# Kernel optimization log

Hardware: AMD Instinct MI355X
Metric: run time of the kernel (lower is better)

Reference implementation:

```python
import jax, jax.numpy as jnp
import numpy as np

N = 1_000_000        # points
V = 200_000          # occupied voxels
B = 4                # scans per batch
NUM_CLASSES = 20
DIM_POINT = 4
EPS = 1e-5


def bn(x, g, b):
    # eval-mode BatchNorm1d with running_mean=0, running_var=1
    return x * (g / jnp.sqrt(1.0 + EPS)) + b


def _lin(key, fi, fo):
    # kaiming-normal init, bias-free Linear stored as [in, out]
    return jax.random.normal(key, (fi, fo), jnp.float32) * np.sqrt(2.0 / fi)


def setup_inputs() -> dict:
    key = jax.random.key(0)
    ks = jax.random.split(key, 20)
    batch_ids = (jnp.arange(N) * B // N).astype(jnp.float32)[:, None]
    coords = jax.random.normal(ks[0], (N, DIM_POINT), jnp.float32)
    points = jnp.concatenate([batch_ids, coords], axis=1)           # [N, 1+dim_point]
    pv_ids = jax.random.randint(ks[1], (N,), 0, V, jnp.int64)       # point -> voxel
    ones, zeros = jnp.ones, jnp.zeros
    return {
        'points': points, 'point_voxel_ids': pv_ids,
        # point encoder: 4->32->64->32, each Linear(no bias)+BN+ReLU
        'pe_w1': _lin(ks[2], DIM_POINT, 32), 'pe_g1': ones(32), 'pe_b1': zeros(32),
        'pe_w2': _lin(ks[3], 32, 64),        'pe_g2': ones(64), 'pe_b2': zeros(64),
        'pe_w3': _lin(ks[4], 64, 32),        'pe_g3': ones(32), 'pe_b3': zeros(32),
        # voxel encoder (SparseUnet simplified to per-voxel 32->32->32)
        've_w1': _lin(ks[5], 32, 32), 've_g1': ones(32), 've_b1': zeros(32),
        've_w2': _lin(ks[6], 32, 32), 've_g2': ones(32), 've_b2': zeros(32),
        # fusion encoder: 64->64
        'fu_w': _lin(ks[7], 64, 64), 'fu_g': ones(64), 'fu_b': zeros(64),
        # FlattenSELayer: 64 -> 64//16 -> 64 with biases
        'se_w1': _lin(ks[8], 64, 4),  'se_b1': zeros(4),
        'se_w2': _lin(ks[9], 4, 64),  'se_b2': zeros(64),
        # main classifier 64->32->num_classes
        'cls_w1': _lin(ks[10], 64, 32), 'cls_g1': ones(32), 'cls_b1': zeros(32),
        'cls_w2': _lin(ks[11], 32, NUM_CLASSES),
        # aux classifier 32->32->num_classes
        'aux_w1': _lin(ks[12], 32, 32), 'aux_g1': ones(32), 'aux_b1': zeros(32),
        'aux_w2': _lin(ks[13], 32, NUM_CLASSES),
    }


def reference(points, point_voxel_ids,
              pe_w1, pe_g1, pe_b1, pe_w2, pe_g2, pe_b2, pe_w3, pe_g3, pe_b3,
              ve_w1, ve_g1, ve_b1, ve_w2, ve_g2, ve_b2,
              fu_w, fu_g, fu_b, se_w1, se_b1, se_w2, se_b2,
              cls_w1, cls_g1, cls_b1, cls_w2,
              aux_w1, aux_g1, aux_b1, aux_w2):
    batch_ids = points[:, 0].astype(jnp.int32)
    pv = point_voxel_ids.astype(jnp.int32)
    x = points[:, 1:]
    # point encoder
    pf = jax.nn.relu(bn(x @ pe_w1, pe_g1, pe_b1))
    pf = jax.nn.relu(bn(pf @ pe_w2, pe_g2, pe_b2))
    pf = jax.nn.relu(bn(pf @ pe_w3, pe_g3, pe_b3))               # [N,32]
    # voxel_max_pooling: point -> voxel scatter-max (empty voxels -> 0)
    vox = jax.ops.segment_max(pf, pv, num_segments=V)
    vox = jnp.where(jnp.isfinite(vox), vox, 0.0)                 # [V,32]
    # voxel encoder (SparseUnet stand-in); v1 is the aux feature tap
    v1 = jax.nn.relu(bn(vox @ ve_w1, ve_g1, ve_b1))              # [V,32]
    vf = jax.nn.relu(bn(v1 @ ve_w2, ve_g2, ve_b2))               # [V,32]
    # voxel_to_point gather + fusion
    pvf = vf[pv]                                                  # [N,32]
    fused = jnp.concatenate([pvf, pf], axis=1)                   # [N,64]
    fused = jax.nn.relu(bn(fused @ fu_w, fu_g, fu_b))
    # FlattenSELayer: per-scan mean -> gate -> residual scale
    sums = jax.ops.segment_sum(fused, batch_ids, num_segments=B)
    cnts = jax.ops.segment_sum(jnp.ones((fused.shape[0], 1), fused.dtype), batch_ids, num_segments=B)
    mean = sums / jnp.maximum(cnts, 1.0)                         # [B,64]
    gate = jax.nn.sigmoid(jax.nn.relu(mean @ se_w1 + se_b1) @ se_w2 + se_b2)
    fused = fused + fused * gate[batch_ids]
    # heads (dropout is identity at inference)
    out = jax.nn.relu(bn(fused @ cls_w1, cls_g1, cls_b1)) @ cls_w2      # [N,C]
    aux_out = jax.nn.relu(bn(v1 @ aux_w1, aux_g1, aux_b1)) @ aux_w2     # [V,C]
    return out, aux_out
```

## Files before the change

### kernel.cpp

```cpp
#include <hip/hip_runtime.h>
#include <hip/hip_bf16.h>

#define NPTS 1000000
#define NVOX 200000
#define NCLS 20

typedef __hip_bfloat16 bf16;
typedef __attribute__((ext_vector_type(8))) short bf16x8_t;
typedef __attribute__((ext_vector_type(4))) float f32x4_t;
#define MFMA16(a, b, c) __builtin_amdgcn_mfma_f32_16x16x32_bf16(a, b, c, 0, 0, 0)

constexpr size_t L_PV   = 0;
constexpr size_t L_BID  = L_PV + NPTS;
constexpr size_t L_CNT  = L_BID + NPTS;
constexpr size_t L_BSUM = L_CNT + NVOX;
constexpr size_t L_BCNT = L_BSUM + 2048;
constexpr size_t L_GATE = L_BCNT + 4;
constexpr size_t L_OFFS = L_GATE + 256;
constexpr size_t L_BS1  = L_OFFS + NVOX;
constexpr size_t L_BB   = L_BS1 + 256;
constexpr size_t L_IDX  = L_BB + 256;
constexpr size_t L_IOR  = L_IDX + NPTS;
constexpr size_t L_W    = L_IOR + NPTS;
constexpr int O_PE1W = 0;      constexpr int O_PE1B = 128;
constexpr int O_PE2W = 160;    constexpr int O_PE2B = 2208;
constexpr int O_PE3W = 2272;   constexpr int O_PE3B = 4320;
constexpr int O_VE1W = 4352;   constexpr int O_VE1B = 5376;
constexpr int O_VE2W = 5408;   constexpr int O_VE2B = 6432;
constexpr int O_FUW  = 6464;   constexpr int O_FUB  = 10560;
constexpr int O_SE1W = 10624;  constexpr int O_SE1B = 10880;
constexpr int O_SE2W = 10884;  constexpr int O_SE2B = 11140;
constexpr int O_CLS1W = 11204; constexpr int O_CLS1B = 13252;
constexpr int O_CLS2W = 13284;
constexpr int O_AUX1W = 13924; constexpr int O_AUX1B = 14948;
constexpr int O_AUX2W = 14980;
constexpr int W_TOTAL = 15620;
constexpr size_t L_WT  = L_W + W_TOTAL;
constexpr int WT_FU = 0;
constexpr int WT_C1 = 4096;
constexpr int WT_C2 = 6144;
constexpr int WT_2H = 7168;
constexpr int WT_2L = 9216;
constexpr int WT_3H = 11264;
constexpr int WT_3L = 13312;
constexpr int WT_C1B = 15360;
constexpr int WT_U16 = 15360 + 8192;
constexpr size_t L_PFQ = L_WT + WT_U16 / 2;
constexpr size_t L_VFP = L_PFQ + (size_t)NPTS * 16;
static_assert((L_PFQ * 4) % 16 == 0, "pfq alignment");
static_assert((L_VFP * 4) % 16 == 0, "vfp alignment");

static __device__ __forceinline__ float b2f(bf16 v) { return __bfloat162float(v); }
static __device__ __forceinline__ float us2f(unsigned short u) { return __uint_as_float((unsigned)u << 16); }
static __device__ __forceinline__ unsigned short f2us(float f) {
    unsigned u = __float_as_uint(f);
    u += 0x7fffu + ((u >> 16) & 1u);
    return (unsigned short)(u >> 16);
}
static __device__ __forceinline__ unsigned pack2(float a, float b) {
    return (unsigned)f2us(a) | ((unsigned)f2us(b) << 16);
}
static __device__ __forceinline__ void unpack2(unsigned u, float& a, float& b) {
    a = __uint_as_float(u << 16);
    b = __uint_as_float(u & 0xffff0000u);
}
static __device__ __forceinline__ float rdf(const void* p, size_t idx, int fp32) {
    return fp32 ? ((const float*)p)[idx] : b2f(((const bf16*)p)[idx]);
}
static __device__ __forceinline__ int detect_fp32(const void* pts_raw) {
    const unsigned short* ptsu = (const unsigned short*)pts_raw;
    return (ptsu[1] == 0 && ptsu[11] == 0) ? 1 : 0;
}
static __device__ __forceinline__ int detect_i64(const void* pv_raw) {
    const unsigned* pvu = (const unsigned*)pv_raw;
    return (pvu[1] == 0 && pvu[3] == 0 && pvu[5] == 0 && pvu[7] == 0) ? 1 : 0;
}

template <int K, int M, bool RELU, bool BIAS>
static __device__ __forceinline__ void dense(const float* __restrict__ x, float* __restrict__ y,
                                             const float* __restrict__ w, const float* __restrict__ b) {
#pragma unroll
    for (int j = 0; j < M; ++j) {
        float a = BIAS ? b[j] : 0.f;
#pragma unroll
        for (int k = 0; k < K; ++k) a = fmaf(x[k], w[k * M + j], a);
        y[j] = RELU ? fmaxf(a, 0.f) : a;
    }
}

static __device__ __forceinline__ int block_excl_scan(int v, int t) {
    __shared__ int sh[2][256];
    int cur = 0;
    sh[0][t] = v; __syncthreads();
#pragma unroll
    for (int off = 1; off < 256; off <<= 1) {
        int val = sh[cur][t];
        if (t >= off) val += sh[cur][t - off];
        sh[cur ^ 1][t] = val; __syncthreads();
        cur ^= 1;
    }
    return sh[cur][t] - v;
}

struct WPtrs {
    const void *pe_w1, *pe_g1, *pe_b1, *pe_w2, *pe_g2, *pe_b2, *pe_w3, *pe_g3, *pe_b3;
    const void *ve_w1, *ve_g1, *ve_b1, *ve_w2, *ve_g2, *ve_b2;
    const void *fu_w, *fu_g, *fu_b;
    const void *se_w1, *se_b1, *se_w2, *se_b2;
    const void *cls_w1, *cls_g1, *cls_b1, *cls_w2;
    const void *aux_w1, *aux_g1, *aux_b1, *aux_w2;
};

static __device__ void foldw(float* d, const void* w, const void* g, int K, int M, int fp32) {
    const float INV = 0.9999950000374997f;
    for (int idx = threadIdx.x; idx < K * M; idx += 256)
        d[idx] = rdf(w, idx, fp32) * (rdf(g, idx % M, fp32) * INV);
}
static __device__ void cpv(float* d, const void* s, int n, int fp32) {
    for (int idx = threadIdx.x; idx < n; idx += 256) d[idx] = rdf(s, idx, fp32);
}

__global__ void k0_prep(WPtrs p, const void* __restrict__ pts_raw, float* __restrict__ W,
                        unsigned short* __restrict__ WT) {
    int f = detect_fp32(pts_raw);
    foldw(W + O_PE1W, p.pe_w1, p.pe_g1, 4, 32, f);   cpv(W + O_PE1B, p.pe_b1, 32, f);
    foldw(W + O_PE2W, p.pe_w2, p.pe_g2, 32, 64, f);  cpv(W + O_PE2B, p.pe_b2, 64, f);
    foldw(W + O_PE3W, p.pe_w3, p.pe_g3, 64, 32, f);  cpv(W + O_PE3B, p.pe_b3, 32, f);
    foldw(W + O_VE1W, p.ve_w1, p.ve_g1, 32, 32, f);  cpv(W + O_VE1B, p.ve_b1, 32, f);
    foldw(W + O_VE2W, p.ve_w2, p.ve_g2, 32, 32, f);  cpv(W + O_VE2B, p.ve_b2, 32, f);
    foldw(W + O_FUW,  p.fu_w,  p.fu_g,  64, 64, f);  cpv(W + O_FUB,  p.fu_b, 64, f);
    cpv(W + O_SE1W, p.se_w1, 256, f);  cpv(W + O_SE1B, p.se_b1, 4, f);
    cpv(W + O_SE2W, p.se_w2, 256, f);  cpv(W + O_SE2B, p.se_b2, 64, f);
    foldw(W + O_CLS1W, p.cls_w1, p.cls_g1, 64, 32, f); cpv(W + O_CLS1B, p.cls_b1, 32, f);
    cpv(W + O_CLS2W, p.cls_w2, 640, f);
    foldw(W + O_AUX1W, p.aux_w1, p.aux_g1, 32, 32, f); cpv(W + O_AUX1B, p.aux_b1, 32, f);
    cpv(W + O_AUX2W, p.aux_w2, 640, f);
    __syncthreads();
    unsigned short* wtfu = WT + WT_FU;
    unsigned short* wtc1 = WT + WT_C1;
    unsigned short* wtc2 = WT + WT_C2;
    unsigned short* wt2h = WT + WT_2H;
    unsigned short* wt2l = WT + WT_2L;
    unsigned short* wt3h = WT + WT_3H;
    unsigned short* wt3l = WT + WT_3L;
    for (int idx = threadIdx.x; idx < 4096; idx += 256) {
        int n = idx >> 6, k = idx & 63;
        wtfu[idx] = f2us(W[O_FUW + k * 64 + n]);
    }
    for (int idx = threadIdx.x; idx < 2048; idx += 256) {
        int n = idx >> 6, k = idx & 63;
        wtc1[idx] = f2us(W[O_CLS1W + k * 32 + n]);
    }
    for (int idx = threadIdx.x; idx < 1024; idx += 256) {
        int n = idx >> 5, k = idx & 31;
        wtc2[idx] = (n < NCLS) ? f2us(W[O_CLS2W + k * NCLS + n]) : (unsigned short)0;
    }
    for (int idx = threadIdx.x; idx < 2048; idx += 256) {
        int n = idx >> 5, k = idx & 31;
        float v = W[O_PE2W + k * 64 + n];
        unsigned short hi = f2us(v);
        wt2h[idx] = hi;
        wt2l[idx] = f2us(v - us2f(hi));
    }
    for (int idx = threadIdx.x; idx < 2048; idx += 256) {
        int n = idx >> 6, k = idx & 63;
        float v = W[O_PE3W + k * 32 + n];
        unsigned short hi = f2us(v);
        wt3h[idx] = hi;
        wt3l[idx] = f2us(v - us2f(hi));
    }
}

__global__ __launch_bounds__(256) void k_scan1(const int* __restrict__ cnt, int* __restrict__ bs) {
    int t = threadIdx.x;
    int base = blockIdx.x * 1024 + t * 4;
    int s = 0;
#pragma unroll
    for (int k = 0; k < 4; ++k) { int idx = base + k; if (idx < NVOX) s += cnt[idx]; }
    __shared__ int red[256];
    red[t] = s; __syncthreads();
    for (int off = 128; off > 0; off >>= 1) { if (t < off) red[t] += red[t + off]; __syncthreads(); }
    if (t == 0) bs[blockIdx.x] = red[0];
}

__global__ __launch_bounds__(256) void k_scan2(const int* __restrict__ bs, int* __restrict__ bb, int nb) {
    int t = threadIdx.x;
    int v = (t < nb) ? bs[t] : 0;
    int e = block_excl_scan(v, t);
    bb[t] = e;
}

__global__ __launch_bounds__(256) void k_scan3(const int* __restrict__ cnt, const int* __restrict__ bb,
                                               int* __restrict__ offs) {
    int t = threadIdx.x;
    int base = blockIdx.x * 1024 + t * 4;
    int c[4]; int s = 0;
#pragma unroll
    for (int k = 0; k < 4; ++k) { int idx = base + k; c[k] = (idx < NVOX) ? cnt[idx] : 0; s += c[k]; }
    int run = bb[blockIdx.x] + block_excl_scan(s, t);
#pragma unroll
    for (int k = 0; k < 4; ++k) {
        int idx = base + k;
        if (idx < NVOX) { offs[idx] = run; run += c[k]; }
    }
}

__global__ __launch_bounds__(256) void k1_fused(const void* __restrict__ pts_raw,
                                                const void* __restrict__ pv_raw,
                                                const float* __restrict__ W,
                                                const unsigned short* __restrict__ WT2H,
                                                const unsigned short* __restrict__ WT2L,
                                                const unsigned short* __restrict__ WT3H,
                                                const unsigned short* __restrict__ WT3L,
                                                int* __restrict__ pvN,
                                                int* __restrict__ bidN,
                                                int* __restrict__ cnt,
                                                float* __restrict__ bcnt,
                                                int* __restrict__ rank,
                                                uint4* __restrict__ pf_q) {
    __shared__ __align__(16) unsigned short hth[4][16][72];
    __shared__ __align__(16) unsigned short htl[4][16][72];
    __shared__ __align__(16) unsigned short pt[4][16][40];
    int t = threadIdx.x;
    int lane = t & 63, w = t >> 6;
    int m = lane & 15, quad = lane >> 4;
    int i0 = blockIdx.x * 256;
    int fp32 = detect_fp32(pts_raw), i64 = detect_i64(pv_raw);

    float w1[32], b1[8];
#pragma unroll
    for (int k = 0; k < 4; ++k)
#pragma unroll
        for (int j = 0; j < 8; ++j) w1[k * 8 + j] = W[O_PE1W + k * 32 + quad * 8 + j];
#pragma unroll
    for (int j = 0; j < 8; ++j) b1[j] = W[O_PE1B + quad * 8 + j];
    bf16x8_t b2h[4], b2l[4], b3h[2][2], b3l[2][2];
    float bias2[4], bias3[2];
#pragma unroll
    for (int tn = 0; tn < 4; ++tn) {
        b2h[tn] = *(const bf16x8_t*)(WT2H + (tn * 16 + m) * 32 + quad * 8);
        b2l[tn] = *(const bf16x8_t*)(WT2L + (tn * 16 + m) * 32 + quad * 8);
        bias2[tn] = W[O_PE2B + tn * 16 + m];
    }
#pragma unroll
    for (int tn = 0; tn < 2; ++tn) {
#pragma unroll
        for (int kh = 0; kh < 2; ++kh) {
            b3h[tn][kh] = *(const bf16x8_t*)(WT3H + (tn * 16 + m) * 64 + kh * 32 + quad * 8);
            b3l[tn][kh] = *(const bf16x8_t*)(WT3L + (tn * 16 + m) * 64 + kh * 32 + quad * 8);
        }
        bias3[tn] = W[O_PE3B + tn * 16 + m];
    }
    int nval = NPTS - i0; if (nval > 256) nval = 256;
    int ntiles = (nval - w * 64 >= 64) ? 4 : 0;

#pragma unroll 1
    for (int tt = 0; tt < ntiles; ++tt) {
        int rbase = i0 + w * 64 + tt * 16;
        int arow = rbase + m;
        float4 c;
        c.x = rdf(pts_raw, (size_t)arow * 5 + 1, fp32);
        c.y = rdf(pts_raw, (size_t)arow * 5 + 2, fp32);
        c.z = rdf(pts_raw, (size_t)arow * 5 + 3, fp32);
        c.w = rdf(pts_raw, (size_t)arow * 5 + 4, fp32);
        union { unsigned u[4]; bf16x8_t v; } ah, al;
#pragma unroll
        for (int pp = 0; pp < 4; ++pp) {
            unsigned hu = 0, lu = 0;
#pragma unroll
            for (int s = 0; s < 2; ++s) {
                int j = 2 * pp + s;
                float h = b1[j];
                h = fmaf(c.x, w1[0 * 8 + j], h);
                h = fmaf(c.y, w1[1 * 8 + j], h);
                h = fmaf(c.z, w1[2 * 8 + j], h);
                h = fmaf(c.w, w1[3 * 8 + j], h);
                h = fmaxf(h, 0.f);
                unsigned short hi = f2us(h);
                unsigned short lo = f2us(h - us2f(hi));
                hu |= (unsigned)hi << (16 * s);
                lu |= (unsigned)lo << (16 * s);
            }
            ah.u[pp] = hu; al.u[pp] = lu;
        }
#pragma unroll
        for (int tn = 0; tn < 4; ++tn) {
            f32x4_t acc = {0.f, 0.f, 0.f, 0.f};
            acc = MFMA16(ah.v, b2h[tn], acc);
            acc = MFMA16(ah.v, b2l[tn], acc);
            acc = MFMA16(al.v, b2h[tn], acc);
#pragma unroll
            for (int e = 0; e < 4; ++e) {
                float v = fmaxf(acc[e] + bias2[tn], 0.f);
                unsigned short hi = f2us(v);
                hth[w][quad * 4 + e][tn * 16 + m] = hi;
                htl[w][quad * 4 + e][tn * 16 + m] = f2us(v - us2f(hi));
            }
        }
        bf16x8_t x0h = *(const bf16x8_t*)&hth[w][m][quad * 8];
        bf16x8_t x1h = *(const bf16x8_t*)&hth[w][m][32 + quad * 8];
        bf16x8_t x0l = *(const bf16x8_t*)&htl[w][m][quad * 8];
        bf16x8_t x1l = *(const bf16x8_t*)&htl[w][m][32 + quad * 8];
#pragma unroll
        for (int tn = 0; tn < 2; ++tn) {
            f32x4_t acc = {0.f, 0.f, 0.f, 0.f};
            acc = MFMA16(x0h, b3h[tn][0], acc);
            acc = MFMA16(x1h, b3h[tn][1], acc);
            acc = MFMA16(x0h, b3l[tn][0], acc);
            acc = MFMA16(x1h, b3l[tn][1], acc);
            acc = MFMA16(x0l, b3h[tn][0], acc);
            acc = MFMA16(x1l, b3h[tn][1], acc);
#pragma unroll
            for (int e = 0; e < 4; ++e)
                pt[w][quad * 4 + e][tn * 16 + m] = f2us(fmaxf(acc[e] + bias3[tn], 0.f));
        }
        uint4 q = *(const uint4*)&pt[w][m][quad * 8];
        pf_q[(size_t)arow * 4 + quad] = q;
    }

    int i = i0 + t;
    bool valid = t < nval;
    int b = 0, rk = 0;
    if (valid) {
        b = (int)rdf(pts_raw, (size_t)i * 5, fp32);
        bidN[i] = b;
        int v = i64 ? (int)((const long long*)pv_raw)[i] : ((const int*)pv_raw)[i];
        pvN[i] = v;
        rk = atomicAdd(&cnt[v], 1);
    }
    __shared__ int sb0, sflag;
    if (t == 0) { sb0 = b; sflag = 1; }
    __syncthreads();
    if (valid && b != sb0) sflag = 0;
    __syncthreads();
    if (sflag) {
        if (t == 0) atomicAdd(&bcnt[sb0], (float)nval);
    } else if (valid) {
        atomicAdd(&bcnt[b], 1.f);
    }
    if (valid) rank[i] = rk;
}

__global__ __launch_bounds__(256) void k_sidx(const int* __restrict__ pv,
                                              const int* __restrict__ rank,
                                              const int* __restrict__ offs,
                                              int* __restrict__ idxs) {
    int i = blockIdx.x * 256 + threadIdx.x;
    if (i >= NPTS) return;
    idxs[offs[pv[i]] + rank[i]] = i;
}

__global__ __launch_bounds__(256) void k_voxmlp(const int* __restrict__ offs, const int* __restrict__ cnt,
                                                const int* __restrict__ idxs,
                                                const uint4* __restrict__ pf_q,
                                                const float* __restrict__ W,
                                                const void* __restrict__ pts_raw,
                                                uint4* __restrict__ vfp,
                                                void* __restrict__ outbase) {
    int v = blockIdx.x * 256 + threadIdx.x;
    if (v >= NVOX) return;
    int of32 = detect_fp32(pts_raw);
    float mx[32];
#pragma unroll
    for (int c = 0; c < 32; ++c) mx[c] = 0.f;
    int s = offs[v], n = cnt[v];
    for (int p = 0; p < n; ++p) {
        int j = idxs[s + p];
        size_t base = (size_t)j * 4;
#pragma unroll
        for (int t = 0; t < 4; ++t) {
            uint4 q = pf_q[base + t];
            float a, b;
            unpack2(q.x, a, b); mx[8*t+0] = fmaxf(mx[8*t+0], a); mx[8*t+1] = fmaxf(mx[8*t+1], b);
            unpack2(q.y, a, b); mx[8*t+2] = fmaxf(mx[8*t+2], a); mx[8*t+3] = fmaxf(mx[8*t+3], b);
            unpack2(q.z, a, b); mx[8*t+4] = fmaxf(mx[8*t+4], a); mx[8*t+5] = fmaxf(mx[8*t+5], b);
            unpack2(q.w, a, b); mx[8*t+6] = fmaxf(mx[8*t+6], a); mx[8*t+7] = fmaxf(mx[8*t+7], b);
        }
    }
    float v1[32], vf[32], a1[32], o[20];
    dense<32, 32, true, true>(mx, v1, W + O_VE1W, W + O_VE1B);
    dense<32, 32, true, true>(v1, vf, W + O_VE2W, W + O_VE2B);
    uint4 vq[4];
#pragma unroll
    for (int t = 0; t < 4; ++t)
        vq[t] = make_uint4(pack2(vf[8*t+0], vf[8*t+1]), pack2(vf[8*t+2], vf[8*t+3]),
                           pack2(vf[8*t+4], vf[8*t+5]), pack2(vf[8*t+6], vf[8*t+7]));
    for (int p = 0; p < n; ++p) {
        int j = idxs[s + p];
        uint4* d = vfp + (size_t)j * 4;
        d[0] = vq[0]; d[1] = vq[1]; d[2] = vq[2]; d[3] = vq[3];
    }
    dense<32, 32, true, true>(v1, a1, W + O_AUX1W, W + O_AUX1B);
    dense<32, 20, false, false>(a1, o, W + O_AUX2W, nullptr);
    if (of32) {
        float* auxf = (float*)outbase + (size_t)NPTS * NCLS + (size_t)v * NCLS;
#pragma unroll
        for (int t = 0; t < NCLS; ++t) __builtin_nontemporal_store(o[t], auxf + t);
    } else {
        unsigned* auxu = (unsigned*)((bf16*)outbase + (size_t)NPTS * NCLS);
#pragma unroll
        for (int t = 0; t < 10; ++t) __builtin_nontemporal_store(pack2(o[2*t], o[2*t+1]), auxu + (size_t)v * 10 + t);
    }
}

__global__ __launch_bounds__(256) void k3_mfma(const int* __restrict__ bid,
                                               const uint4* __restrict__ pf_q,
                                               const uint4* __restrict__ vfp,
                                               const float* __restrict__ W,
                                               const unsigned short* __restrict__ WTfu,
                                               float* __restrict__ bsum8) {
    __shared__ int sbid[256];
    __shared__ float red[4][64];
    __shared__ int sflag;
    int t = threadIdx.x;
    int i0 = blockIdx.x * 256;
    int nval = NPTS - i0; if (nval > 256) nval = 256;
    if (t < nval) sbid[t] = bid[i0 + t];
    if (t == 0) sflag = (bid[i0] == bid[i0 + nval - 1]) ? 1 : 0;

    int lane = t & 63, w = t >> 6;
    int m = lane & 15, quad = lane >> 4;
    bf16x8_t bw0[4], bw1[4];
    float bias[4];
#pragma unroll
    for (int tn = 0; tn < 4; ++tn) {
        bw0[tn] = *(const bf16x8_t*)(WTfu + (tn * 16 + m) * 64 + quad * 8);
        bw1[tn] = *(const bf16x8_t*)(WTfu + (tn * 16 + m) * 64 + 32 + quad * 8);
        bias[tn] = W[O_FUB + tn * 16 + m];
    }
    __syncthreads();
    int uni = sflag;
    int b0 = sbid[0];
    int rep = (blockIdx.x & 7) * 256;
    int ntiles = (nval - w * 64 >= 64) ? 4 : 0;

    float csum[4] = {0.f, 0.f, 0.f, 0.f};
#pragma unroll
    for (int tt = 0; tt < 4; ++tt) {
        if (tt >= ntiles) break;
        int rbase = i0 + w * 64 + tt * 16;
        int arow = rbase + m;
        uint4 va = vfp[(size_t)arow * 4 + quad];
        uint4 vb = pf_q[(size_t)arow * 4 + quad];
        bf16x8_t a0 = *(bf16x8_t*)&va;
        bf16x8_t a1 = *(bf16x8_t*)&vb;
        float f[4][4];
#pragma unroll
        for (int tn = 0; tn < 4; ++tn) {
            f32x4_t acc = {0.f, 0.f, 0.f, 0.f};
            acc = MFMA16(a0, bw0[tn], acc);
            acc = MFMA16(a1, bw1[tn], acc);
#pragma unroll
            for (int e = 0; e < 4; ++e) f[tn][e] = fmaxf(acc[e] + bias[tn], 0.f);
        }
        if (uni) {
#pragma unroll
            for (int tn = 0; tn < 4; ++tn) {
                float s = f[tn][0] + f[tn][1] + f[tn][2] + f[tn][3];
                s += __shfl_xor(s, 16);
                s += __shfl_xor(s, 32);
                csum[tn] += s;
            }
        } else {
#pragma unroll
            for (int tn = 0; tn < 4; ++tn)
#pragma unroll
                for (int e = 0; e < 4; ++e)
                    atomicAdd(&bsum8[rep + sbid[rbase - i0 + quad * 4 + e] * 64 + tn * 16 + m], f[tn][e]);
        }
    }
    if (uni) {
        float mine = quad == 0 ? csum[0] : quad == 1 ? csum[1] : quad == 2 ? csum[2] : csum[3];
        red[w][quad * 16 + m] = mine;
        __syncthreads();
        if (t < 64) {
            float s = red[0][t] + red[1][t] + red[2][t] + red[3][t];
            atomicAdd(&bsum8[rep + b0 * 64 + t], s);
        }
    }
}

__global__ void k4_gate(const float* __restrict__ bsum8, const float* __restrict__ bcnt,
                        const float* __restrict__ W, const unsigned short* __restrict__ WTc1,
                        float* __restrict__ gate, unsigned short* __restrict__ WTc1B) {
    __shared__ float m[4][64];
    __shared__ float hid[4][4];
    __shared__ float gl[256];
    int tid = threadIdx.x, b = tid >> 6, c = tid & 63;
    float s = 0.f;
#pragma unroll
    for (int r = 0; r < 8; ++r) s += bsum8[r * 256 + tid];
    m[b][c] = s / fmaxf(bcnt[b], 1.f);
    __syncthreads();
    if (c < 4) {
        const float* w = W + O_SE1W;
        float a = (W + O_SE1B)[c];
        for (int k = 0; k < 64; ++k) a = fmaf(m[b][k], w[k * 4 + c], a);
        hid[b][c] = fmaxf(a, 0.f);
    }
    __syncthreads();
    const float* w2 = W + O_SE2W;
    float g = (W + O_SE2B)[c];
#pragma unroll
    for (int h = 0; h < 4; ++h) g = fmaf(hid[b][h], w2[h * 64 + c], g);
    g = 1.f + 1.f / (1.f + expf(-g));
    gate[tid] = g;
    gl[tid] = g;
    __syncthreads();
    for (int idx = tid; idx < 8192; idx += 256) {
        int bb = idx >> 11, j = idx & 2047, k = j & 63;
        WTc1B[idx] = f2us(us2f(WTc1[j]) * gl[bb * 64 + k]);
    }
}

__global__ __launch_bounds__(256) void k5_mfma(const int* __restrict__ bid,
                                               const uint4* __restrict__ pf_q,
                                               const uint4* __restrict__ vfp,
                                               const float* __restrict__ W,
                                               const unsigned short* __restrict__ WTfu,
                                               const unsigned short* __restrict__ WTc1,
                                               const unsigned short* __restrict__ WTc1B,
                                               const unsigned short* __restrict__ WTc2,
                                               const float* __restrict__ gate,
                                               const void* __restrict__ pts_raw,
                                               void* __restrict__ out) {
    __shared__ float sg[256];
    __shared__ int sbid[256];
    __shared__ int sflag;
    __shared__ __align__(16) unsigned short ft[4][16][72];
    __shared__ __align__(16) unsigned short ht[4][16][40];
    __shared__ float ot[4][16][20];
    int t = threadIdx.x;
    int i0 = blockIdx.x * 256;
    int nval = NPTS - i0; if (nval > 256) nval = 256;
    sg[t] = gate[t];
    if (t < nval) sbid[t] = bid[i0 + t];
    if (t == 0) sflag = (bid[i0] == bid[i0 + nval - 1]) ? 1 : 0;

    int lane = t & 63, w = t >> 6;
    int m = lane & 15, quad = lane >> 4;
    bf16x8_t bfu0[4], bfu1[4];
    float biasfu[4];
#pragma unroll
    for (int tn = 0; tn < 4; ++tn) {
        bfu0[tn] = *(const bf16x8_t*)(WTfu + (tn * 16 + m) * 64 + quad * 8);
        bfu1[tn] = *(const bf16x8_t*)(WTfu + (tn * 16 + m) * 64 + 32 + quad * 8);
        biasfu[tn] = W[O_FUB + tn * 16 + m];
    }
    __syncthreads();
    int uni = sflag;
    int b0 = sbid[0];
    int of32 = detect_fp32(pts_raw);
    int ntiles = (nval - w * 64 >= 64) ? 4 : 0;

    const unsigned short* c1base = uni ? (WTc1B + b0 * 2048) : WTc1;
    bf16x8_t bc10[2], bc11[2], bc2[2];
    float biasc1[2];
#pragma unroll
    for (int tn = 0; tn < 2; ++tn) {
        bc10[tn] = *(const bf16x8_t*)(c1base + (tn * 16 + m) * 64 + quad * 8);
        bc11[tn] = *(const bf16x8_t*)(c1base + (tn * 16 + m) * 64 + 32 + quad * 8);
        bc2[tn]  = *(const bf16x8_t*)(WTc2 + (tn * 16 + m) * 32 + quad * 8);
        biasc1[tn] = W[O_CLS1B + tn * 16 + m];
    }

#pragma unroll 1
    for (int tt = 0; tt < ntiles; ++tt) {
        int rbase = i0 + w * 64 + tt * 16;
        int arow = rbase + m;
        uint4 va = vfp[(size_t)arow * 4 + quad];
        uint4 vb = pf_q[(size_t)arow * 4 + quad];
        bf16x8_t a0 = *(bf16x8_t*)&va;
        bf16x8_t a1 = *(bf16x8_t*)&vb;
#pragma unroll
        for (int tn = 0; tn < 4; ++tn) {
            f32x4_t acc = {0.f, 0.f, 0.f, 0.f};
            acc = MFMA16(a0, bfu0[tn], acc);
            acc = MFMA16(a1, bfu1[tn], acc);
#pragma unroll
            for (int e = 0; e < 4; ++e) {
                float fv = fmaxf(acc[e] + biasfu[tn], 0.f);
                if (!uni) fv *= sg[sbid[rbase - i0 + quad * 4 + e] * 64 + tn * 16 + m];
                ft[w][quad * 4 + e][tn * 16 + m] = f2us(fv);
            }
        }
        bf16x8_t c0 = *(const bf16x8_t*)&ft[w][m][quad * 8];
        bf16x8_t c1 = *(const bf16x8_t*)&ft[w][m][32 + quad * 8];
#pragma unroll
        for (int tn = 0; tn < 2; ++tn) {
            f32x4_t acc = {0.f, 0.f, 0.f, 0.f};
            acc = MFMA16(c0, bc10[tn], acc);
            acc = MFMA16(c1, bc11[tn], acc);
#pragma unroll
            for (int e = 0; e < 4; ++e)
                ht[w][quad * 4 + e][tn * 16 + m] = f2us(fmaxf(acc[e] + biasc1[tn], 0.f));
        }
        bf16x8_t d0 = *(const bf16x8_t*)&ht[w][m][quad * 8];
#pragma unroll
        for (int tn = 0; tn < 2; ++tn) {
            f32x4_t acc = {0.f, 0.f, 0.f, 0.f};
            acc = MFMA16(d0, bc2[tn], acc);
            int c = tn * 16 + m;
            if (c < NCLS) {
#pragma unroll
                for (int e = 0; e < 4; ++e) ot[w][quad * 4 + e][c] = acc[e];
            }
        }
        if (of32) {
            float* of = (float*)out + (size_t)rbase * NCLS;
#pragma unroll
            for (int k = 0; k < 5; ++k) {
                int idx = k * 64 + lane;
                __builtin_nontemporal_store(((const float*)ot[w])[idx], of + idx);
            }
        } else {
            unsigned* ow = (unsigned*)((unsigned short*)out + (size_t)rbase * NCLS);
#pragma unroll
            for (int k = 0; k < 3; ++k) {
                int idx = k * 64 + lane;
                if (idx < 160) {
                    int p = idx / 10, c2 = idx - p * 10;
                    __builtin_nontemporal_store(pack2(ot[w][p][2 * c2], ot[w][p][2 * c2 + 1]), ow + idx);
                }
            }
        }
    }
}

extern "C" void kernel_launch(void* const* d_in, const int* in_sizes, int n_in,
                              void* d_out, int out_size, void* d_ws, size_t ws_size,
                              hipStream_t stream) {
    WPtrs p;
    p.pe_w1 = d_in[2];  p.pe_g1 = d_in[3];  p.pe_b1 = d_in[4];
    p.pe_w2 = d_in[5];  p.pe_g2 = d_in[6];  p.pe_b2 = d_in[7];
    p.pe_w3 = d_in[8];  p.pe_g3 = d_in[9];  p.pe_b3 = d_in[10];
    p.ve_w1 = d_in[11]; p.ve_g1 = d_in[12]; p.ve_b1 = d_in[13];
    p.ve_w2 = d_in[14]; p.ve_g2 = d_in[15]; p.ve_b2 = d_in[16];
    p.fu_w  = d_in[17]; p.fu_g  = d_in[18]; p.fu_b  = d_in[19];
    p.se_w1 = d_in[20]; p.se_b1 = d_in[21];
    p.se_w2 = d_in[22]; p.se_b2 = d_in[23];
    p.cls_w1 = d_in[24]; p.cls_g1 = d_in[25]; p.cls_b1 = d_in[26];
    p.cls_w2 = d_in[27];
    p.aux_w1 = d_in[28]; p.aux_g1 = d_in[29]; p.aux_b1 = d_in[30];
    p.aux_w2 = d_in[31];

    float* base = (float*)d_ws;
    int*   pvN  = (int*)(base + L_PV);
    int*   bidN = (int*)(base + L_BID);
    int*   cnt  = (int*)(base + L_CNT);
    float* bsum8 = base + L_BSUM;
    float* bcnt = base + L_BCNT;
    float* gate = base + L_GATE;
    int*   offs = (int*)(base + L_OFFS);
    int*   bs1  = (int*)(base + L_BS1);
    int*   bb   = (int*)(base + L_BB);
    int*   rank = (int*)(base + L_IDX);
    int*   idxs = (int*)(base + L_IOR);
    float* W    = base + L_W;
    unsigned short* WT = (unsigned short*)(base + L_WT);
    unsigned short* wtfu = WT + WT_FU;
    unsigned short* wtc1 = WT + WT_C1;
    unsigned short* wtc2 = WT + WT_C2;
    unsigned short* wt2h = WT + WT_2H;
    unsigned short* wt2l = WT + WT_2L;
    unsigned short* wt3h = WT + WT_3H;
    unsigned short* wt3l = WT + WT_3L;
    unsigned short* wtc1b = WT + WT_C1B;
    uint4* pf_q = (uint4*)(base + L_PFQ);
    uint4* vfp  = (uint4*)(base + L_VFP);

    constexpr int NBP = (NPTS + 255) / 256;
    constexpr int NBV = (NVOX + 255) / 256;
    constexpr int NBS = (NVOX + 1023) / 1024;
    constexpr int NBM = (NPTS + 255) / 256;

    hipMemsetAsync(cnt, 0, (NVOX + 2048 + 4) * sizeof(float), stream);
    k0_prep<<<1, 256, 0, stream>>>(p, d_in[0], W, WT);
    k1_fused<<<NBM, 256, 0, stream>>>(d_in[0], d_in[1], W, wt2h, wt2l, wt3h, wt3l,
                                      pvN, bidN, cnt, bcnt, rank, pf_q);
    k_scan1<<<NBS, 256, 0, stream>>>(cnt, bs1);
    k_scan2<<<1, 256, 0, stream>>>(bs1, bb, NBS);
    k_scan3<<<NBS, 256, 0, stream>>>(cnt, bb, offs);
    k_sidx<<<NBP, 256, 0, stream>>>(pvN, rank, offs, idxs);
    k_voxmlp<<<NBV, 256, 0, stream>>>(offs, cnt, idxs, pf_q, W, d_in[0], vfp, d_out);
    k3_mfma<<<NBM, 256, 0, stream>>>(bidN, pf_q, vfp, W, wtfu, bsum8);
    k4_gate<<<1, 256, 0, stream>>>(bsum8, bcnt, W, wtc1, gate, wtc1b);
    k5_mfma<<<NBM, 256, 0, stream>>>(bidN, pf_q, vfp, W,
                                     wtfu, wtc1, wtc1b, wtc2, gate, d_in[0], d_out);
}
```

Baseline: 558.0 us.

## Split voxel MLP across four lanes per voxel with shuffle reductions

The voxel kernel now assigns four threads to each voxel. Each lane max-pools and scatters one 16-byte quarter of the 32-channel feature, computes a partial or sliced share of the dense layers, and combines partial sums with xor shuffles. This cuts per-thread register use and serial gather length, and makes gathers and scatters more coalesced across lanes. In exchange it launches four times as many threads, adds shuffle traffic, and repeats the idx loads in every lane.

```diff
diff --git a/kernel.cpp b/kernel.cpp
--- a/kernel.cpp
+++ b/kernel.cpp
@@ -357,49 +357,88 @@
                                                 const void* __restrict__ pts_raw,
                                                 uint4* __restrict__ vfp,
                                                 void* __restrict__ outbase) {
-    int v = blockIdx.x * 256 + threadIdx.x;
+    int tid = blockIdx.x * 256 + threadIdx.x;
+    int v = tid >> 2, q = tid & 3;
     if (v >= NVOX) return;
     int of32 = detect_fp32(pts_raw);
-    float mx[32];
-#pragma unroll
-    for (int c = 0; c < 32; ++c) mx[c] = 0.f;
+    float mx[8];
+#pragma unroll
+    for (int c = 0; c < 8; ++c) mx[c] = 0.f;
     int s = offs[v], n = cnt[v];
     for (int p = 0; p < n; ++p) {
         int j = idxs[s + p];
-        size_t base = (size_t)j * 4;
-#pragma unroll
-        for (int t = 0; t < 4; ++t) {
-            uint4 q = pf_q[base + t];
-            float a, b;
-            unpack2(q.x, a, b); mx[8*t+0] = fmaxf(mx[8*t+0], a); mx[8*t+1] = fmaxf(mx[8*t+1], b);
-            unpack2(q.y, a, b); mx[8*t+2] = fmaxf(mx[8*t+2], a); mx[8*t+3] = fmaxf(mx[8*t+3], b);
-            unpack2(q.z, a, b); mx[8*t+4] = fmaxf(mx[8*t+4], a); mx[8*t+5] = fmaxf(mx[8*t+5], b);
-            unpack2(q.w, a, b); mx[8*t+6] = fmaxf(mx[8*t+6], a); mx[8*t+7] = fmaxf(mx[8*t+7], b);
-        }
-    }
-    float v1[32], vf[32], a1[32], o[20];
-    dense<32, 32, true, true>(mx, v1, W + O_VE1W, W + O_VE1B);
-    dense<32, 32, true, true>(v1, vf, W + O_VE2W, W + O_VE2B);
-    uint4 vq[4];
-#pragma unroll
-    for (int t = 0; t < 4; ++t)
-        vq[t] = make_uint4(pack2(vf[8*t+0], vf[8*t+1]), pack2(vf[8*t+2], vf[8*t+3]),
-                           pack2(vf[8*t+4], vf[8*t+5]), pack2(vf[8*t+6], vf[8*t+7]));
+        uint4 qq = pf_q[(size_t)j * 4 + q];
+        float a, b;
+        unpack2(qq.x, a, b); mx[0] = fmaxf(mx[0], a); mx[1] = fmaxf(mx[1], b);
+        unpack2(qq.y, a, b); mx[2] = fmaxf(mx[2], a); mx[3] = fmaxf(mx[3], b);
+        unpack2(qq.z, a, b); mx[4] = fmaxf(mx[4], a); mx[5] = fmaxf(mx[5], b);
+        unpack2(qq.w, a, b); mx[6] = fmaxf(mx[6], a); mx[7] = fmaxf(mx[7], b);
+    }
+    float v1[32];
+#pragma unroll
+    for (int jj = 0; jj < 32; ++jj) {
+        float a = 0.f;
+#pragma unroll
+        for (int kk = 0; kk < 8; ++kk) a = fmaf(mx[kk], W[O_VE1W + (q * 8 + kk) * 32 + jj], a);
+        v1[jj] = a;
+    }
+#pragma unroll
+    for (int jj = 0; jj < 32; ++jj) {
+        v1[jj] += __shfl_xor(v1[jj], 1);
+        v1[jj] += __shfl_xor(v1[jj], 2);
+        v1[jj] = fmaxf(v1[jj] + W[O_VE1B + jj], 0.f);
+    }
+    float vf8[8];
+#pragma unroll
+    for (int i2 = 0; i2 < 8; ++i2) {
+        int jj = q * 8 + i2;
+        float a = W[O_VE2B + jj];
+#pragma unroll
+        for (int k = 0; k < 32; ++k) a = fmaf(v1[k], W[O_VE2W + k * 32 + jj], a);
+        vf8[i2] = fmaxf(a, 0.f);
+    }
+    uint4 myq = make_uint4(pack2(vf8[0], vf8[1]), pack2(vf8[2], vf8[3]),
+                           pack2(vf8[4], vf8[5]), pack2(vf8[6], vf8[7]));
     for (int p = 0; p < n; ++p) {
         int j = idxs[s + p];
-        uint4* d = vfp + (size_t)j * 4;
-        d[0] = vq[0]; d[1] = vq[1]; d[2] = vq[2]; d[3] = vq[3];
-    }
-    dense<32, 32, true, true>(v1, a1, W + O_AUX1W, W + O_AUX1B);
-    dense<32, 20, false, false>(a1, o, W + O_AUX2W, nullptr);
+        vfp[(size_t)j * 4 + q] = myq;
+    }
+    float a18[8];
+#pragma unroll
+    for (int i2 = 0; i2 < 8; ++i2) {
+        int jj = q * 8 + i2;
+        float a = W[O_AUX1B + jj];
+#pragma unroll
+        for (int k = 0; k < 32; ++k) a = fmaf(v1[k], W[O_AUX1W + k * 32 + jj], a);
+        a18[i2] = fmaxf(a, 0.f);
+    }
+    float o[20];
+#pragma unroll
+    for (int j = 0; j < 20; ++j) {
+        float a = 0.f;
+#pragma unroll
+        for (int kk = 0; kk < 8; ++kk) a = fmaf(a18[kk], W[O_AUX2W + (q * 8 + kk) * 20 + j], a);
+        o[j] = a;
+    }
+#pragma unroll
+    for (int j = 0; j < 20; ++j) {
+        o[j] += __shfl_xor(o[j], 1);
+        o[j] += __shfl_xor(o[j], 2);
+    }
     if (of32) {
         float* auxf = (float*)outbase + (size_t)NPTS * NCLS + (size_t)v * NCLS;
 #pragma unroll
-        for (int t = 0; t < NCLS; ++t) __builtin_nontemporal_store(o[t], auxf + t);
+        for (int r = 0; r < 5; ++r) {
+            int j = q + r * 4;
+            __builtin_nontemporal_store(o[j], auxf + j);
+        }
     } else {
-        unsigned* auxu = (unsigned*)((bf16*)outbase + (size_t)NPTS * NCLS);
-#pragma unroll
-        for (int t = 0; t < 10; ++t) __builtin_nontemporal_store(pack2(o[2*t], o[2*t+1]), auxu + (size_t)v * 10 + t);
+        unsigned* auxu = (unsigned*)((bf16*)outbase + (size_t)NPTS * NCLS) + (size_t)v * 10;
+#pragma unroll
+        for (int r = 0; r < 3; ++r) {
+            int j = q + r * 4;
+            if (j < 10) __builtin_nontemporal_store(pack2(o[2 * j], o[2 * j + 1]), auxu + j);
+        }
     }
 }
 
@@ -670,7 +709,7 @@
     uint4* vfp  = (uint4*)(base + L_VFP);
 
     constexpr int NBP = (NPTS + 255) / 256;
-    constexpr int NBV = (NVOX + 255) / 256;
+    constexpr int NBV4 = (NVOX * 4 + 255) / 256;
     constexpr int NBS = (NVOX + 1023) / 1024;
     constexpr int NBM = (NPTS + 255) / 256;
 
@@ -682,7 +721,7 @@
     k_scan2<<<1, 256, 0, stream>>>(bs1, bb, NBS);
     k_scan3<<<NBS, 256, 0, stream>>>(cnt, bb, offs);
     k_sidx<<<NBP, 256, 0, stream>>>(pvN, rank, offs, idxs);
-    k_voxmlp<<<NBV, 256, 0, stream>>>(offs, cnt, idxs, pf_q, W, d_in[0], vfp, d_out);
+    k_voxmlp<<<NBV4, 256, 0, stream>>>(offs, cnt, idxs, pf_q, W, d_in[0], vfp, d_out);
     k3_mfma<<<NBM, 256, 0, stream>>>(bidN, pf_q, vfp, W, wtfu, bsum8);
     k4_gate<<<1, 256, 0, stream>>>(bsum8, bcnt, W, wtc1, gate, wtc1b);
     k5_mfma<<<NBM, 256, 0, stream>>>(bidN, pf_q, vfp, W,
```

Result: slower. 670.2 us (+20.1%).
